# Optimization experiments

Hardware: AMD Instinct MI355X
Metric: run time of the kernel (lower is better)

## Reference

```python
import jax, jax.numpy as jnp
import numpy as np

EMBED = 1024
HEADS = 16
HEAD_DIM = EMBED // HEADS
N, SEQ = 8, 1024


def setup_inputs() -> dict:
    key = jax.random.key(0)
    ks = jax.random.split(key, 8)
    s = 1.0 / np.sqrt(HEAD_DIM)
    so = 1.0 / np.sqrt(EMBED)
    return {
        "values": jax.random.normal(ks[0], (N, SEQ, EMBED), jnp.float32),
        "keys": jax.random.normal(ks[1], (N, SEQ, EMBED), jnp.float32),
        "query": jax.random.normal(ks[2], (N, SEQ, EMBED), jnp.float32),
        "mask": jnp.ones((N, 1, 1, SEQ), jnp.int32),
        "Wv": jax.random.normal(ks[3], (HEAD_DIM, HEAD_DIM), jnp.float32) * s,
        "Wk": jax.random.normal(ks[4], (HEAD_DIM, HEAD_DIM), jnp.float32) * s,
        "Wq": jax.random.normal(ks[5], (HEAD_DIM, HEAD_DIM), jnp.float32) * s,
        "Wo": jax.random.normal(ks[6], (EMBED, EMBED), jnp.float32) * so,
        "bo": jnp.zeros((EMBED,), jnp.float32),
    }


def reference(values, keys, query, mask, Wv, Wk, Wq, Wo, bo):
    n, ql = query.shape[0], query.shape[1]
    # split heads: (N, L, H, D)
    v = values.reshape(n, -1, HEADS, HEAD_DIM)
    k = keys.reshape(n, -1, HEADS, HEAD_DIM)
    q = query.reshape(n, -1, HEADS, HEAD_DIM)
    # per-head linear projections (nn.Linear, no bias): x @ W^T
    v = jnp.einsum("nlhd,ed->nlhe", v, Wv)
    k = jnp.einsum("nlhd,ed->nlhe", k, Wk)
    q = jnp.einsum("nlhd,ed->nlhe", q, Wq)
    # scores: (N, H, Q, K)
    energy = jnp.einsum("nqhd,nkhd->nhqk", q, k)
    energy = jnp.where(mask == 0, jnp.float32(-1e10), energy)
    attn = jax.nn.softmax(energy / jnp.sqrt(jnp.float32(EMBED)), axis=-1)
    out = jnp.einsum("nhqk,nkhd->nqhd", attn, v).reshape(n, ql, EMBED)
    return out @ Wo.T + bo
```

## Files before the change

### kernel.cpp

```cpp
#include <hip/hip_runtime.h>
#include <hip/hip_bf16.h>
#include <stdint.h>

typedef unsigned short u16;
typedef __bf16 bf16_t;
typedef bf16_t bf16x8 __attribute__((ext_vector_type(8)));
typedef float f32x4 __attribute__((ext_vector_type(4)));
typedef float f32x16 __attribute__((ext_vector_type(16)));

#define MFMA16(a, b, c) __builtin_amdgcn_mfma_f32_16x16x32_bf16((a), (b), (c), 0, 0, 0)
#define MFMA32(a, b, c) __builtin_amdgcn_mfma_f32_32x32x16_bf16((a), (b), (c), 0, 0, 0)

#define NBATCH 8
#define SEQL 1024
#define EMB 1024
#define NHEAD 16
#define HD 64

static __device__ __forceinline__ u16 f2b(float f) {
  bf16_t b = (bf16_t)f;
  return __builtin_bit_cast(u16, b);
}

union V16 { uint4 u; bf16x8 b; };

static __device__ __forceinline__ bf16x8 ldb8(const u16* p) {
  V16 v; v.u = *(const uint4*)p; return v.b;
}

static __device__ __forceinline__ bf16x8 cvt8(const float* p) {
  float4 a = *(const float4*)p;
  float4 b = *(const float4*)(p + 4);
  bf16x8 r;
  r[0] = (bf16_t)a.x; r[1] = (bf16_t)a.y; r[2] = (bf16_t)a.z; r[3] = (bf16_t)a.w;
  r[4] = (bf16_t)b.x; r[5] = (bf16_t)b.y; r[6] = (bf16_t)b.z; r[7] = (bf16_t)b.w;
  return r;
}

static __device__ __forceinline__ void gload16(const void* g, void* l) {
  __builtin_amdgcn_global_load_lds((__attribute__((address_space(1))) void*)(uintptr_t)g,
                                   (__attribute__((address_space(3))) void*)l, 16, 0, 0);
}

static __device__ __forceinline__ unsigned cvtpk(float lo, float hi) {
  unsigned r;
  asm("v_cvt_pk_bf16_f32 %0, %1, %2" : "=v"(r) : "v"(lo), "v"(hi));
  return r;
}

static __device__ __forceinline__ f32x16 zero16() {
  f32x16 z;
#pragma unroll
  for (int i = 0; i < 16; ++i) z[i] = 0.f;
  return z;
}

__global__ __launch_bounds__(256) void k_wcvt(const float* __restrict__ Wo, u16* __restrict__ Wob) {
  int i = (blockIdx.x * 256 + threadIdx.x) * 4;
  float4 f = *(const float4*)(Wo + i);
  unsigned p0 = (unsigned)f2b(f.x) | ((unsigned)f2b(f.y) << 16);
  unsigned p1 = (unsigned)f2b(f.z) | ((unsigned)f2b(f.w) << 16);
  uint2 o; o.x = p0; o.y = p1;
  *(uint2*)(Wob + i) = o;
}

__global__ __launch_bounds__(256) void k_proj3(const float* __restrict__ Xv, const float* __restrict__ Xk,
                                               const float* __restrict__ Xq, const float* __restrict__ Wv,
                                               const float* __restrict__ Wk, const float* __restrict__ Wq,
                                               u16* __restrict__ Vt, u16* __restrict__ Kp, u16* __restrict__ Qp) {
  __shared__ __align__(16) u16 xs[16 * 1024];
  __shared__ __align__(16) u16 obuf[4][16 * 72];
  __shared__ __align__(16) u16 ob2[4][1024];
  int z = blockIdx.z;
  const float* X = (z == 0) ? Xv : (z == 1) ? Xk : Xq;
  const float* W = (z == 0) ? Wv : (z == 1) ? Wk : Wq;
  u16* Out = (z == 0) ? Vt : (z == 1) ? Kp : Qp;
  int vmode = (z == 0);
  float qs = (z == 2) ? 0.04508422f : 1.0f;

  int gr0 = blockIdx.x * 16;
  int n = gr0 >> 10, l0 = gr0 & 1023;
  int tid = threadIdx.x, w = tid >> 6, lane = tid & 63;
  int lr = lane & 15, lg = lane >> 4;

  bf16x8 bw[4][2];
#pragma unroll
  for (int c = 0; c < 4; ++c)
#pragma unroll
    for (int kk = 0; kk < 2; ++kk)
      bw[c][kk] = cvt8(W + (lr + 16 * c) * HD + kk * 32 + lg * 8);

#pragma unroll
  for (int i = 0; i < 8; ++i) {
    int m = i * 256 + tid;
    int row = m >> 7, cc = m & 127;
    V16 v; v.b = cvt8(X + (size_t)gr0 * 1024 + (size_t)m * 8);
    *(uint4*)(xs + row * 1024 + ((cc ^ (row & 7)) * 8)) = v.u;
  }
  __syncthreads();

#pragma unroll 1
  for (int h4 = 0; h4 < 4; ++h4) {
    int h = w * 4 + h4;
    int nh = n * 16 + h;
    bf16x8 a0 = ldb8(xs + lr * 1024 + (((h * 8 + 0 + lg) ^ (lr & 7)) * 8));
    bf16x8 a1 = ldb8(xs + lr * 1024 + (((h * 8 + 4 + lg) ^ (lr & 7)) * 8));
    f32x4 acc[4];
#pragma unroll
    for (int c = 0; c < 4; ++c) {
      f32x4 zz = {0.f, 0.f, 0.f, 0.f};
      zz = MFMA16(a0, bw[c][0], zz);
      zz = MFMA16(a1, bw[c][1], zz);
      acc[c] = zz;
    }
    if (!vmode) {
      u16* ob = obuf[w];
#pragma unroll
      for (int c = 0; c < 4; ++c)
#pragma unroll
        for (int rr = 0; rr < 4; ++rr)
          ob[(lg * 4 + rr) * 72 + lr + 16 * c] = f2b(acc[c][rr] * qs);
      int orow = lane >> 2, oseg = lane & 3;
      uint4 v0 = *(const uint4*)(ob + orow * 72 + oseg * 16);
      uint4 v1 = *(const uint4*)(ob + orow * 72 + oseg * 16 + 8);
      u16* dst = Out + ((size_t)nh * SEQL + l0 + orow) * HD + oseg * 16;
      *(uint4*)dst = v0;
      *(uint4*)(dst + 8) = v1;
    } else {
      u16* o2 = ob2[w];
#pragma unroll
      for (int c = 0; c < 4; ++c) {
        ushort4 p;
        p.x = f2b(acc[c][0]); p.y = f2b(acc[c][1]); p.z = f2b(acc[c][2]); p.w = f2b(acc[c][3]);
        *(ushort4*)(o2 + (lg >> 1) * 512 + (lr + 16 * c) * 8 + (lg & 1) * 4) = p;
      }
      int lb0 = l0 >> 3;
#pragma unroll
      for (int lbi = 0; lbi < 2; ++lbi) {
        uint4 vv = *(const uint4*)(o2 + lbi * 512 + lane * 8);
        *(uint4*)(Out + (size_t)nh * 65536 + (size_t)(lb0 + lbi) * 512 + lane * 8) = vv;
      }
    }
  }
}

__global__ __launch_bounds__(256, 2) void k_attn2(const u16* __restrict__ Qp, const u16* __restrict__ Kp,
                                                  const u16* __restrict__ Vt, const int* __restrict__ mask,
                                                  u16* __restrict__ AO) {
  __shared__ __align__(16) u16 SMEM[2][8192];
  __shared__ unsigned long long mkb[16];
  __shared__ __align__(16) float winv[4][2][32];

  int nh = blockIdx.x;
  int n = nh >> 4, h = nh & 15;
  int tid = threadIdx.x, w = tid >> 6, lane = tid & 63;
  int q = lane & 31, hi = lane >> 5;
  int q0w = blockIdx.y * 256 + w * 64;

  bf16x8 bq[2][4];
#pragma unroll
  for (int g = 0; g < 2; ++g) {
    const u16* qbase = Qp + ((size_t)nh * SEQL + q0w + g * 32 + q) * HD + hi * 8;
#pragma unroll
    for (int kk = 0; kk < 4; ++kk) bq[g][kk] = ldb8(qbase + kk * 16);
  }

  const u16* gK = Kp + (size_t)nh * SEQL * HD;
  const u16* gV = Vt + (size_t)nh * HD * SEQL;
  int sr = lane >> 3, sslot = lane & 7;

  auto STAGE = [&](int b, int t) {
#pragma unroll
    for (int j = 0; j < 2; ++j) {
      int r = 16 * w + 8 * j + sr;
      int slot = sslot ^ (r & 7);
      gload16(gK + ((size_t)(t * 64 + r)) * HD + slot * 8,
              &SMEM[b][w * 1024 + j * 512]);
      gload16(gV + (size_t)(t * 8 + slot) * 512 + r * 8,
              &SMEM[b][4096 + w * 1024 + j * 512]);
    }
  };

  STAGE(0, 0);
#pragma unroll 1
  for (int t = w; t < 16; t += 4) {
    int mv = mask[n * SEQL + t * 64 + lane];
    unsigned long long b = __ballot(mv != 0);
    if (lane == 0) mkb[t] = b;
  }
  __syncthreads();

  f32x16 oacc[2][2];
  oacc[0][0] = zero16(); oacc[0][1] = zero16();
  oacc[1][0] = zero16(); oacc[1][1] = zero16();
  float lsum0 = 0.f, lsum1 = 0.f;
  int buf = 0;

#pragma unroll 1
  for (int kt = 0; kt < 16; ++kt) {
    if (kt < 15) STAGE(buf ^ 1, kt + 1);
    const u16* KB = &SMEM[buf][0];
    const u16* VB = &SMEM[buf][4096];
    unsigned long long mb = mkb[kt];

#pragma unroll
    for (int c = 0; c < 2; ++c) {
      f32x16 s0 = zero16(), s1 = zero16();
      {
        int row = 32 * c + q;
        int swz = (row & 7) << 3;
        const u16* kr = KB + row * 64;
        __builtin_amdgcn_s_setprio(1);
#pragma unroll
        for (int kk = 0; kk < 4; ++kk) {
          bf16x8 ak = ldb8(kr + ((16 * kk + 8 * hi) ^ swz));
          s0 = MFMA32(ak, bq[0][kk], s0);
          s1 = MFMA32(ak, bq[1][kk], s1);
        }
        __builtin_amdgcn_s_setprio(0);
      }

#pragma unroll
      for (int rr = 0; rr < 16; ++rr) {
        s0[rr] = __builtin_amdgcn_exp2f(s0[rr]);
        s1[rr] = __builtin_amdgcn_exp2f(s1[rr]);
      }
      if (mb != ~0ull) {
#pragma unroll
        for (int rr = 0; rr < 16; ++rr) {
          int kpos = 32 * c + 4 * hi + (rr & 3) + 8 * (rr >> 2);
          if (!((mb >> kpos) & 1)) { s0[rr] = 0.f; s1[rr] = 0.f; }
        }
      }
#pragma unroll
      for (int rr = 0; rr < 16; ++rr) { lsum0 += s0[rr]; lsum1 += s1[rr]; }

      bf16x8 pa0[2], pa1[2];
#pragma unroll
      for (int p2 = 0; p2 < 2; ++p2) {
        unsigned a0 = cvtpk(s0[8 * p2 + 0], s0[8 * p2 + 1]);
        unsigned a1 = cvtpk(s0[8 * p2 + 2], s0[8 * p2 + 3]);
        unsigned b0 = cvtpk(s0[8 * p2 + 4], s0[8 * p2 + 5]);
        unsigned b1 = cvtpk(s0[8 * p2 + 6], s0[8 * p2 + 7]);
        auto r0 = __builtin_amdgcn_permlane32_swap(a0, b0, false, false);
        auto r1 = __builtin_amdgcn_permlane32_swap(a1, b1, false, false);
        union { unsigned u[4]; bf16x8 v; } pu;
        pu.u[0] = r0[0]; pu.u[1] = r1[0]; pu.u[2] = r0[1]; pu.u[3] = r1[1];
        pa0[p2] = pu.v;
        unsigned c0 = cvtpk(s1[8 * p2 + 0], s1[8 * p2 + 1]);
        unsigned c1 = cvtpk(s1[8 * p2 + 2], s1[8 * p2 + 3]);
        unsigned d0 = cvtpk(s1[8 * p2 + 4], s1[8 * p2 + 5]);
        unsigned d1 = cvtpk(s1[8 * p2 + 6], s1[8 * p2 + 7]);
        auto r2 = __builtin_amdgcn_permlane32_swap(c0, d0, false, false);
        auto r3 = __builtin_amdgcn_permlane32_swap(c1, d1, false, false);
        union { unsigned u[4]; bf16x8 v; } pv;
        pv.u[0] = r2[0]; pv.u[1] = r3[0]; pv.u[2] = r2[1]; pv.u[3] = r3[1];
        pa1[p2] = pv.v;
      }

      __builtin_amdgcn_s_setprio(1);
#pragma unroll
      for (int cp = 0; cp < 2; ++cp) {
        int row = 32 * cp + q;
        int swz = (row & 7) << 3;
        const u16* vr = VB + row * 64;
#pragma unroll
        for (int p2 = 0; p2 < 2; ++p2) {
          int t = 2 * c + p2;
          bf16x8 vb = ldb8(vr + ((16 * t + 8 * hi) ^ swz));
          oacc[0][cp] = MFMA32(pa0[p2], vb, oacc[0][cp]);
          oacc[1][cp] = MFMA32(pa1[p2], vb, oacc[1][cp]);
        }
      }
      __builtin_amdgcn_s_setprio(0);
    }
    __syncthreads();
    buf ^= 1;
  }

  float t0 = lsum0 + __shfl_xor(lsum0, 32);
  float t1 = lsum1 + __shfl_xor(lsum1, 32);
  if (!hi) { winv[w][0][q] = 1.0f / t0; winv[w][1][q] = 1.0f / t1; }

  u16* ob = &SMEM[0][0] + w * 2560;
  int orow = lane >> 1, ohalf = lane & 1;
#pragma unroll
  for (int g = 0; g < 2; ++g) {
    float iq[16];
#pragma unroll
    for (int w2 = 0; w2 < 4; ++w2) {
      float4 f = *(const float4*)&winv[w][g][8 * w2 + 4 * hi];
      iq[4 * w2 + 0] = f.x; iq[4 * w2 + 1] = f.y; iq[4 * w2 + 2] = f.z; iq[4 * w2 + 3] = f.w;
    }
#pragma unroll
    for (int cp = 0; cp < 2; ++cp)
#pragma unroll
      for (int rr = 0; rr < 16; ++rr) {
        int qr = (rr & 3) + 8 * (rr >> 2) + 4 * hi;
        ob[qr * 80 + 32 * cp + q] = f2b(oacc[g][cp][rr] * iq[rr]);
      }
    __builtin_amdgcn_s_barrier();
    const u16* srcp = ob + orow * 80 + ohalf * 32;
    uint4 v0 = *(const uint4*)srcp;
    uint4 v1 = *(const uint4*)(srcp + 8);
    uint4 v2 = *(const uint4*)(srcp + 16);
    uint4 v3 = *(const uint4*)(srcp + 24);
    u16* dst = AO + ((size_t)(n * SEQL + q0w + g * 32 + orow)) * EMB + h * HD + ohalf * 32;
    *(uint4*)dst = v0;
    *(uint4*)(dst + 8) = v1;
    *(uint4*)(dst + 16) = v2;
    *(uint4*)(dst + 24) = v3;
  }
}

__global__ __launch_bounds__(256) void k_out(const u16* __restrict__ AO, const u16* __restrict__ Wob,
                                             const float* __restrict__ bo, float* __restrict__ Y) {
  __shared__ __align__(16) u16 As[2][4096];
  __shared__ __align__(16) u16 Bs[2][4096];
  int n0 = blockIdx.x * 128, m0 = blockIdx.y * 128;
  int tid = threadIdx.x, w = tid >> 6, lane = tid & 63;
  int lr = lane & 15, lg = lane >> 4;
  int wr = w >> 1, wc = w & 1;
  int srow = lane >> 2, sseg = lane & 3;

  auto STAGE = [&](int b, int kb) {
#pragma unroll
    for (int j = 0; j < 2; ++j) {
      int row = 32 * w + 16 * j + srow;
      gload16(AO + (size_t)(m0 + row) * EMB + kb * 32 + sseg * 8, &As[b][w * 1024 + j * 512]);
      gload16(Wob + (size_t)(n0 + row) * EMB + kb * 32 + sseg * 8, &Bs[b][w * 1024 + j * 512]);
    }
  };

  f32x4 acc[4][4] = {};
  STAGE(0, 0);
  __syncthreads();
  int buf = 0;
#pragma unroll 1
  for (int kb = 0; kb < 32; ++kb) {
    if (kb < 31) STAGE(buf ^ 1, kb + 1);
    bf16x8 a[4], b[4];
#pragma unroll
    for (int mi = 0; mi < 4; ++mi)
      a[mi] = ldb8(&As[buf][(wr * 64 + mi * 16 + lr) * 32 + lg * 8]);
#pragma unroll
    for (int ni = 0; ni < 4; ++ni)
      b[ni] = ldb8(&Bs[buf][(wc * 64 + ni * 16 + lr) * 32 + lg * 8]);
#pragma unroll
    for (int mi = 0; mi < 4; ++mi)
#pragma unroll
      for (int ni = 0; ni < 4; ++ni)
        acc[mi][ni] = MFMA16(a[mi], b[ni], acc[mi][ni]);
    __syncthreads();
    buf ^= 1;
  }
#pragma unroll
  for (int ni = 0; ni < 4; ++ni) {
    float bov = bo[n0 + wc * 64 + ni * 16 + lr];
#pragma unroll
    for (int mi = 0; mi < 4; ++mi) {
#pragma unroll
      for (int rr = 0; rr < 4; ++rr) {
        int row = m0 + wr * 64 + mi * 16 + lg * 4 + rr;
        int col = n0 + wc * 64 + ni * 16 + lr;
        Y[(size_t)row * EMB + col] = acc[mi][ni][rr] + bov;
      }
    }
  }
}

extern "C" void kernel_launch(void* const* d_in, const int* in_sizes, int n_in,
                              void* d_out, int out_size, void* d_ws, size_t ws_size,
                              hipStream_t stream) {
  (void)in_sizes; (void)n_in; (void)out_size; (void)ws_size;
  const float* values = (const float*)d_in[0];
  const float* keys   = (const float*)d_in[1];
  const float* query  = (const float*)d_in[2];
  const int*   mask   = (const int*)d_in[3];
  const float* Wv = (const float*)d_in[4];
  const float* Wk = (const float*)d_in[5];
  const float* Wq = (const float*)d_in[6];
  const float* Wo = (const float*)d_in[7];
  const float* bo = (const float*)d_in[8];
  float* out = (float*)d_out;

  u16* ws  = (u16*)d_ws;
  u16* Qp  = ws;
  u16* Kp  = ws + (size_t)8 * 1024 * 1024;
  u16* Vt  = ws + (size_t)16 * 1024 * 1024;
  u16* AO  = ws + (size_t)24 * 1024 * 1024;
  u16* Wob = ws + (size_t)32 * 1024 * 1024;

  k_wcvt<<<dim3(1024), dim3(256), 0, stream>>>(Wo, Wob);
  k_proj3<<<dim3(512, 1, 3), dim3(256), 0, stream>>>(values, keys, query, Wv, Wk, Wq, Vt, Kp, Qp);
  k_attn2<<<dim3(128, 4), dim3(256), 0, stream>>>(Qp, Kp, Vt, mask, AO);
  k_out<<<dim3(8, 64), dim3(256), 0, stream>>>(AO, Wob, bo, out);
}
```

Baseline: 106.8 us.

## Double K-tile depth in attention and output GEMM, add XCD-aware block mapping

The attention kernel now stages 128-key tiles instead of 64, halving the number of loop iterations and barriers. The V tile gets a wider XOR swizzle, and the row-sum reduction becomes a tree. The output GEMM now stages 64-wide K slices with an XOR swizzle and raises MFMA priority. It also uses a 1D grid remapped so that each XCD works on a contiguous band of rows, for better L2 locality. The extra LDS per block may reduce occupancy in the attention kernel, which declares launch bounds of 2 blocks.

```diff
diff --git a/kernel.cpp b/kernel.cpp
--- a/kernel.cpp
+++ b/kernel.cpp
@@ -53,6 +53,13 @@
 #pragma unroll
   for (int i = 0; i < 16; ++i) z[i] = 0.f;
   return z;
+}
+
+static __device__ __forceinline__ float sum16(const f32x16& s) {
+  float a0 = s[0] + s[1], a1 = s[2] + s[3], a2 = s[4] + s[5], a3 = s[6] + s[7];
+  float a4 = s[8] + s[9], a5 = s[10] + s[11], a6 = s[12] + s[13], a7 = s[14] + s[15];
+  float b0 = a0 + a1, b1 = a2 + a3, b2 = a4 + a5, b3 = a6 + a7;
+  return (b0 + b1) + (b2 + b3);
 }
 
 __global__ __launch_bounds__(256) void k_wcvt(const float* __restrict__ Wo, u16* __restrict__ Wob) {
@@ -147,7 +154,7 @@
 __global__ __launch_bounds__(256, 2) void k_attn2(const u16* __restrict__ Qp, const u16* __restrict__ Kp,
                                                   const u16* __restrict__ Vt, const int* __restrict__ mask,
                                                   u16* __restrict__ AO) {
-  __shared__ __align__(16) u16 SMEM[2][8192];
+  __shared__ __align__(16) u16 SMEM[2][16384];
   __shared__ unsigned long long mkb[16];
   __shared__ __align__(16) float winv[4][2][32];
 
@@ -167,17 +174,18 @@
 
   const u16* gK = Kp + (size_t)nh * SEQL * HD;
   const u16* gV = Vt + (size_t)nh * HD * SEQL;
-  int sr = lane >> 3, sslot = lane & 7;
+  int sr8 = lane >> 3, ss8 = lane & 7;
+  int sr4 = lane >> 4, ss16 = lane & 15;
 
   auto STAGE = [&](int b, int t) {
 #pragma unroll
-    for (int j = 0; j < 2; ++j) {
-      int r = 16 * w + 8 * j + sr;
-      int slot = sslot ^ (r & 7);
-      gload16(gK + ((size_t)(t * 64 + r)) * HD + slot * 8,
-              &SMEM[b][w * 1024 + j * 512]);
-      gload16(gV + (size_t)(t * 8 + slot) * 512 + r * 8,
-              &SMEM[b][4096 + w * 1024 + j * 512]);
+    for (int j = 0; j < 4; ++j) {
+      int r = 32 * w + 8 * j + sr8;
+      gload16(gK + ((size_t)(t * 128 + r)) * 64 + ((ss8 ^ (r & 7)) * 8),
+              &SMEM[b][w * 2048 + j * 512]);
+      int d = 16 * w + 4 * j + sr4;
+      gload16(gV + (size_t)(t * 16 + (ss16 ^ (d & 15))) * 512 + d * 8,
+              &SMEM[b][8192 + w * 2048 + j * 512]);
     }
   };
 
@@ -197,14 +205,13 @@
   int buf = 0;
 
 #pragma unroll 1
-  for (int kt = 0; kt < 16; ++kt) {
-    if (kt < 15) STAGE(buf ^ 1, kt + 1);
+  for (int kt = 0; kt < 8; ++kt) {
+    if (kt < 7) STAGE(buf ^ 1, kt + 1);
     const u16* KB = &SMEM[buf][0];
-    const u16* VB = &SMEM[buf][4096];
-    unsigned long long mb = mkb[kt];
-
-#pragma unroll
-    for (int c = 0; c < 2; ++c) {
+    const u16* VB = &SMEM[buf][8192];
+
+#pragma unroll
+    for (int c = 0; c < 4; ++c) {
       f32x16 s0 = zero16(), s1 = zero16();
       {
         int row = 32 * c + q;
@@ -225,15 +232,16 @@
         s0[rr] = __builtin_amdgcn_exp2f(s0[rr]);
         s1[rr] = __builtin_amdgcn_exp2f(s1[rr]);
       }
+      unsigned long long mb = mkb[2 * kt + (c >> 1)];
       if (mb != ~0ull) {
 #pragma unroll
         for (int rr = 0; rr < 16; ++rr) {
-          int kpos = 32 * c + 4 * hi + (rr & 3) + 8 * (rr >> 2);
+          int kpos = 32 * (c & 1) + 4 * hi + (rr & 3) + 8 * (rr >> 2);
           if (!((mb >> kpos) & 1)) { s0[rr] = 0.f; s1[rr] = 0.f; }
         }
       }
-#pragma unroll
-      for (int rr = 0; rr < 16; ++rr) { lsum0 += s0[rr]; lsum1 += s1[rr]; }
+      lsum0 += sum16(s0);
+      lsum1 += sum16(s1);
 
       bf16x8 pa0[2], pa1[2];
 #pragma unroll
@@ -262,12 +270,12 @@
 #pragma unroll
       for (int cp = 0; cp < 2; ++cp) {
         int row = 32 * cp + q;
-        int swz = (row & 7) << 3;
-        const u16* vr = VB + row * 64;
+        int vswz = (row & 15) << 3;
+        const u16* vr = VB + row * 128;
 #pragma unroll
         for (int p2 = 0; p2 < 2; ++p2) {
-          int t = 2 * c + p2;
-          bf16x8 vb = ldb8(vr + ((16 * t + 8 * hi) ^ swz));
+          int tq = 2 * c + p2;
+          bf16x8 vb = ldb8(vr + ((16 * tq + 8 * hi) ^ vswz));
           oacc[0][cp] = MFMA32(pa0[p2], vb, oacc[0][cp]);
           oacc[1][cp] = MFMA32(pa1[p2], vb, oacc[1][cp]);
         }
@@ -315,20 +323,25 @@
 
 __global__ __launch_bounds__(256) void k_out(const u16* __restrict__ AO, const u16* __restrict__ Wob,
                                              const float* __restrict__ bo, float* __restrict__ Y) {
-  __shared__ __align__(16) u16 As[2][4096];
-  __shared__ __align__(16) u16 Bs[2][4096];
-  int n0 = blockIdx.x * 128, m0 = blockIdx.y * 128;
+  __shared__ __align__(16) u16 As[2][8192];
+  __shared__ __align__(16) u16 Bs[2][8192];
+  int g = blockIdx.x;
+  int xcd = g & 7, rr_ = g >> 3;
+  int m0 = (xcd * 8 + (rr_ >> 3)) * 128;
+  int n0 = (rr_ & 7) * 128;
   int tid = threadIdx.x, w = tid >> 6, lane = tid & 63;
   int lr = lane & 15, lg = lane >> 4;
   int wr = w >> 1, wc = w & 1;
-  int srow = lane >> 2, sseg = lane & 3;
+  int sr8 = lane >> 3, ss8 = lane & 7;
 
   auto STAGE = [&](int b, int kb) {
 #pragma unroll
-    for (int j = 0; j < 2; ++j) {
-      int row = 32 * w + 16 * j + srow;
-      gload16(AO + (size_t)(m0 + row) * EMB + kb * 32 + sseg * 8, &As[b][w * 1024 + j * 512]);
-      gload16(Wob + (size_t)(n0 + row) * EMB + kb * 32 + sseg * 8, &Bs[b][w * 1024 + j * 512]);
+    for (int j = 0; j < 4; ++j) {
+      int row = 32 * w + 8 * j + sr8;
+      gload16(AO + (size_t)(m0 + row) * EMB + kb * 64 + ((ss8 ^ (row & 7)) * 8),
+              &As[b][w * 2048 + j * 512]);
+      gload16(Wob + (size_t)(n0 + row) * EMB + kb * 64 + ((ss8 ^ (row & 7)) * 8),
+              &Bs[b][w * 2048 + j * 512]);
     }
   };
 
@@ -337,20 +350,30 @@
   __syncthreads();
   int buf = 0;
 #pragma unroll 1
-  for (int kb = 0; kb < 32; ++kb) {
-    if (kb < 31) STAGE(buf ^ 1, kb + 1);
-    bf16x8 a[4], b[4];
+  for (int kb = 0; kb < 16; ++kb) {
+    if (kb < 15) STAGE(buf ^ 1, kb + 1);
+    bf16x8 a0[4], a1[4], b0[4], b1[4];
+#pragma unroll
+    for (int mi = 0; mi < 4; ++mi) {
+      int row = wr * 64 + mi * 16 + lr;
+      a0[mi] = ldb8(&As[buf][row * 64 + (((0 + lg) ^ (row & 7)) * 8)]);
+      a1[mi] = ldb8(&As[buf][row * 64 + (((4 + lg) ^ (row & 7)) * 8)]);
+    }
+#pragma unroll
+    for (int ni = 0; ni < 4; ++ni) {
+      int row = wc * 64 + ni * 16 + lr;
+      b0[ni] = ldb8(&Bs[buf][row * 64 + (((0 + lg) ^ (row & 7)) * 8)]);
+      b1[ni] = ldb8(&Bs[buf][row * 64 + (((4 + lg) ^ (row & 7)) * 8)]);
+    }
+    __builtin_amdgcn_s_setprio(1);
 #pragma unroll
     for (int mi = 0; mi < 4; ++mi)
-      a[mi] = ldb8(&As[buf][(wr * 64 + mi * 16 + lr) * 32 + lg * 8]);
-#pragma unroll
-    for (int ni = 0; ni < 4; ++ni)
-      b[ni] = ldb8(&Bs[buf][(wc * 64 + ni * 16 + lr) * 32 + lg * 8]);
-#pragma unroll
-    for (int mi = 0; mi < 4; ++mi)
-#pragma unroll
-      for (int ni = 0; ni < 4; ++ni)
-        acc[mi][ni] = MFMA16(a[mi], b[ni], acc[mi][ni]);
+#pragma unroll
+      for (int ni = 0; ni < 4; ++ni) {
+        acc[mi][ni] = MFMA16(a0[mi], b0[ni], acc[mi][ni]);
+        acc[mi][ni] = MFMA16(a1[mi], b1[ni], acc[mi][ni]);
+      }
+    __builtin_amdgcn_s_setprio(0);
     __syncthreads();
     buf ^= 1;
   }
@@ -394,5 +417,5 @@
   k_wcvt<<<dim3(1024), dim3(256), 0, stream>>>(Wo, Wob);
   k_proj3<<<dim3(512, 1, 3), dim3(256), 0, stream>>>(values, keys, query, Wv, Wk, Wq, Vt, Kp, Qp);
   k_attn2<<<dim3(128, 4), dim3(256), 0, stream>>>(Qp, Kp, Vt, mask, AO);
-  k_out<<<dim3(8, 64), dim3(256), 0, stream>>>(AO, Wob, bo, out);
-}
+  k_out<<<dim3(512), dim3(256), 0, stream>>>(AO, Wob, bo, out);
+}
```

After: 136.8 us. 1.28x slower.
